# Kernel optimization log

Hardware: AMD Instinct MI355X
Metric: run time of the kernel (lower is better)

## Reference

```python
import jax, jax.numpy as jnp
import numpy as np

NUM_NODES = 50000
D_IN, D_HID, D_OUT = 128, 128, 40
NUM_EDGES = 800000


def setup_inputs() -> dict:
    key = jax.random.key(0)
    ks = jax.random.split(key, 10)
    x = jax.random.normal(ks[0], (NUM_NODES, D_IN), dtype=jnp.float32)
    edge_index = jax.random.randint(ks[1], (2, NUM_EDGES), 0, NUM_NODES, dtype=jnp.int64)
    # GCNConv weights (lin: in -> out), glorot-style init; bias init zeros per bias_init
    def glorot(k, fan_in, fan_out):
        lim = np.sqrt(6.0 / (fan_in + fan_out)).astype(np.float32)
        return jax.random.uniform(k, (fan_in, fan_out), jnp.float32, -lim, lim)
    W0 = glorot(ks[2], D_IN, D_HID)
    b0 = jnp.zeros((D_HID,), jnp.float32)
    W1 = glorot(ks[3], D_HID, D_HID)
    b1 = jnp.zeros((D_HID,), jnp.float32)
    W2 = glorot(ks[4], D_HID, D_OUT)
    b2 = jnp.zeros((D_OUT,), jnp.float32)
    return {"x": x, "edge_index": edge_index,
            "W0": W0, "b0": b0, "W1": W1, "b1": b1, "W2": W2, "b2": b2}


def _gcn_conv(h, src, dst, W, b):
    # linear projection then gather from source nodes, scatter-add to dest nodes
    hW = h @ W                                   # [N, out]
    msg = jnp.take(hW, src, axis=0)              # [E, out]
    agg = jax.ops.segment_sum(msg, dst, num_segments=NUM_NODES)  # [N, out]
    return agg + b


def reference(x, edge_index, W0, b0, W1, b1, W2, b2):
    src, dst = edge_index[0], edge_index[1]
    h = jax.nn.relu(_gcn_conv(x, src, dst, W0, b0))
    h = jax.nn.relu(_gcn_conv(h, src, dst, W1, b1))
    return _gcn_conv(h, src, dst, W2, b2)
```

## Files before the change

### kernel.cpp

```cpp
#include <hip/hip_runtime.h>

#define NN 50000
#define EE 800000

#define BKT 196
#define GB  334
#define EPB 2396
#define CAPB 6144
#define CAP 5120

typedef unsigned short u16;
typedef unsigned int u32;
typedef __attribute__((ext_vector_type(8))) short short8;
typedef __attribute__((ext_vector_type(4))) float f32x4;
typedef __attribute__((ext_vector_type(4))) unsigned short ushort4v;

__device__ __forceinline__ float b2f(u16 u) {
    return __uint_as_float(((unsigned)u) << 16);
}
__device__ __forceinline__ u16 f2b(float f) {
    unsigned u = __float_as_uint(f);
    return (u16)((u + 0x7FFF + ((u >> 16) & 1)) >> 16);
}

__global__ __launch_bounds__(256) void prep_init(
    const float* __restrict__ W0, const float* __restrict__ W1,
    const float* __restrict__ W2, u16* __restrict__ Wf,
    int* __restrict__ gCur)
{
    const int g = blockIdx.x, t = threadIdx.x;
    if (g == 24) {
        if (t < BKT) gCur[t] = t * CAPB;
        return;
    }
    int u = g * 4 + (t >> 6);
    int set = u >> 5, nt2 = (u >> 2) & 7, kt = u & 3;
    int lane = t & 63;
    const float* W = (set == 0) ? W0 : (set == 1) ? W1 : W2;
    int ld = (set == 2) ? 40 : 128;
    int ncols = (set == 2) ? 40 : 128;
    int n = nt2 * 16 + (lane & 15);
    int kb = kt * 32 + (lane >> 4) * 8;
    u16* dw = Wf + set * 16384 + (size_t)((nt2 * 4 + kt) * 64 + lane) * 8;
#pragma unroll
    for (int j = 0; j < 8; j++) {
        float v = (n < ncols) ? W[(kb + j) * ld + n] : 0.f;
        dw[j] = f2b(v);
    }
}

__global__ __launch_bounds__(256) void scatter_gemm0(
    const int* __restrict__ src, const int* __restrict__ dst,
    int* __restrict__ gCur, u32* __restrict__ pairs,
    const float* __restrict__ A, const u16* __restrict__ Wf,
    u16* __restrict__ out, int N, int E)
{
    __shared__ int cnt[BKT];
    __shared__ int cur[BKT];
    const int t = threadIdx.x;
    if (blockIdx.x < GB) {
        const int g = blockIdx.x;
        for (int b = t; b < BKT; b += 256) cnt[b] = 0;
        __syncthreads();
        const int beg = g * EPB, end = min(E, beg + EPB);
        for (int e = beg + t; e < end; e += 256)
            atomicAdd(&cnt[dst[e] >> 8], 1);
        __syncthreads();
        for (int b = t; b < BKT; b += 256)
            cur[b] = atomicAdd(&gCur[b], cnt[b]);
        __syncthreads();
        for (int e = beg + t; e < end; e += 256) {
            int d = dst[e];
            int pos = atomicAdd(&cur[d >> 8], 1);
            pairs[pos] = ((u32)src[e] << 8) | (u32)(d & 255);
        }
        return;
    }
    const int bx = blockIdx.x - GB;
    const int wave = t >> 6;
    const int lane = t & 63;
    const int m = lane & 15;
    const int q = lane >> 4;
    const int rowBase = bx * 64 + wave * 16;
    const int arow = rowBase + m;
    const bool rowOk = (arow < N);

    short8 af[4];
#pragma unroll
    for (int kt = 0; kt < 4; kt++) {
        if (rowOk) {
            float4 lo = *(const float4*)(A + (size_t)arow * 128 + kt * 32 + q * 8);
            float4 hi = *(const float4*)(A + (size_t)arow * 128 + kt * 32 + q * 8 + 4);
            short8 v;
            v[0] = (short)f2b(lo.x); v[1] = (short)f2b(lo.y);
            v[2] = (short)f2b(lo.z); v[3] = (short)f2b(lo.w);
            v[4] = (short)f2b(hi.x); v[5] = (short)f2b(hi.y);
            v[6] = (short)f2b(hi.z); v[7] = (short)f2b(hi.w);
            af[kt] = v;
        } else {
            af[kt] = (short8)0;
        }
    }

    f32x4 acc[8];
#pragma unroll
    for (int nt = 0; nt < 8; nt++) acc[nt] = (f32x4)0.f;

#pragma unroll
    for (int kt = 0; kt < 4; kt++) {
#pragma unroll
        for (int nt = 0; nt < 8; nt++) {
            short8 bf = *(const short8*)(Wf + (size_t)((nt * 4 + kt) * 64 + lane) * 8);
            acc[nt] = __builtin_amdgcn_mfma_f32_16x16x32_bf16(af[kt], bf, acc[nt], 0, 0, 0);
        }
    }

#pragma unroll
    for (int nt = 0; nt < 8; nt++) {
#pragma unroll
        for (int r = 0; r < 4; r++) {
            int orow = rowBase + q * 4 + r;
            if (orow < N) out[(size_t)orow * 128 + nt * 16 + m] = f2b(acc[nt][r]);
        }
    }
}

__global__ __launch_bounds__(256) void bucket_sort(
    const u32* __restrict__ pairs, const int* __restrict__ gCur,
    int* __restrict__ off, int* __restrict__ csr, int N, int E)
{
    __shared__ int sdeg[256];
    __shared__ int sex[256];
    __shared__ int scur[256];
    __shared__ int stage[CAP];
    const int b = blockIdx.x, t = threadIdx.x;

    int c0 = (t < BKT) ? (gCur[t] - t * CAPB) : 0;
    sex[t] = c0;
    __syncthreads();
    for (int d = 1; d < 256; d <<= 1) {
        int u = (t >= d) ? sex[t - d] : 0;
        __syncthreads();
        sex[t] += u;
        __syncthreads();
    }
    __shared__ int sBase, sCnt;
    if (t == b) { sBase = sex[t] - c0; sCnt = c0; }
    __syncthreads();
    const int base = sBase;
    const int cnt = sCnt;
    const int pbase = b * CAPB;
    __syncthreads();

    sdeg[t] = 0;
    __syncthreads();
    for (int i = t; i < cnt; i += 256)
        atomicAdd(&sdeg[pairs[pbase + i] & 255], 1);
    __syncthreads();

    int v = sdeg[t];
    sex[t] = v;
    __syncthreads();
    for (int d = 1; d < 256; d <<= 1) {
        int u = (t >= d) ? sex[t - d] : 0;
        __syncthreads();
        sex[t] += u;
        __syncthreads();
    }
    const int excl = sex[t] - v;
    const int node = b * 256 + t;
    if (node < N) off[node] = base + excl;
    if (b == BKT - 1 && t == 0) off[N] = E;
    scur[t] = excl;
    __syncthreads();

    if (cnt <= CAP) {
        for (int i = t; i < cnt; i += 256) {
            u32 p = pairs[pbase + i];
            int pos = atomicAdd(&scur[p & 255], 1);
            stage[pos] = (int)(p >> 8);
        }
        __syncthreads();
        for (int i = t; i < cnt; i += 256) csr[base + i] = stage[i];
    } else {
        for (int i = t; i < cnt; i += 256) {
            u32 p = pairs[pbase + i];
            int pos = atomicAdd(&scur[p & 255], 1);
            csr[base + pos] = (int)(p >> 8);
        }
    }
}

template<int NT, int OSTRIDE, int OCOLS>
__global__ __launch_bounds__(512) void agg_gemm_t(
    const u16* __restrict__ val, const int* __restrict__ off,
    const int* __restrict__ csr, const float* __restrict__ bias,
    const u16* __restrict__ Wf, u16* __restrict__ out, int N)
{
    __shared__ u16 A[64][136];
    const int tid = threadIdx.x;
    const int rowBase = blockIdx.x * 64;

    {
        const int c = tid & 15;
        const int nl = tid >> 4;
        float4 bA = *(const float4*)(bias + c * 8);
        float4 bB = *(const float4*)(bias + c * 8 + 4);
        float bb[8] = {bA.x, bA.y, bA.z, bA.w, bB.x, bB.y, bB.z, bB.w};
#pragma unroll
        for (int g = 0; g < 2; g++) {
            const int lrow = g * 32 + nl;
            const int node = rowBase + lrow;
            float a0[8] = {0, 0, 0, 0, 0, 0, 0, 0};
            float a1[8] = {0, 0, 0, 0, 0, 0, 0, 0};
            if (node < N) {
                const int beg = off[node], end = off[node + 1];
                int i = beg;
                for (; i + 3 < end; i += 4) {
                    int s0 = csr[i];
                    int s1 = csr[i + 1];
                    int s2 = csr[i + 2];
                    int s3 = csr[i + 3];
                    short8 v0 = *(const short8*)(val + (size_t)s0 * 128 + c * 8);
                    short8 v1 = *(const short8*)(val + (size_t)s1 * 128 + c * 8);
                    short8 v2 = *(const short8*)(val + (size_t)s2 * 128 + c * 8);
                    short8 v3 = *(const short8*)(val + (size_t)s3 * 128 + c * 8);
#pragma unroll
                    for (int j = 0; j < 8; j++) {
                        a0[j] += b2f((u16)v0[j]) + b2f((u16)v2[j]);
                        a1[j] += b2f((u16)v1[j]) + b2f((u16)v3[j]);
                    }
                }
                for (; i < end; i++) {
                    int s0 = csr[i];
                    short8 v0 = *(const short8*)(val + (size_t)s0 * 128 + c * 8);
#pragma unroll
                    for (int j = 0; j < 8; j++) a0[j] += b2f((u16)v0[j]);
                }
            }
            short8 o;
#pragma unroll
            for (int j = 0; j < 8; j++)
                o[j] = (short)f2b(fmaxf(a0[j] + a1[j] + bb[j], 0.f));
            *(short8*)&A[lrow][c * 8] = o;
        }
    }
    __syncthreads();

    const int wave = tid >> 6;
    const int lane = tid & 63;
    const int m = lane & 15;
    const int q = lane >> 4;
    const int rg = wave & 3;
    const int ch = wave >> 2;
    const int lrow = rg * 16 + m;

    short8 af[4];
#pragma unroll
    for (int kt = 0; kt < 4; kt++)
        af[kt] = *(const short8*)&A[lrow][kt * 32 + q * 8];

    constexpr int NTH = (NT + 1) / 2;
    const int ntB = ch ? NTH : 0;
    const int ntE = ch ? NT : NTH;

    f32x4 acc[NTH];
#pragma unroll
    for (int i = 0; i < NTH; i++) acc[i] = (f32x4)0.f;

#pragma unroll
    for (int kt = 0; kt < 4; kt++) {
        for (int nt = ntB; nt < ntE; nt++) {
            short8 bf = *(const short8*)(Wf + (size_t)((nt * 4 + kt) * 64 + lane) * 8);
            acc[nt - ntB] = __builtin_amdgcn_mfma_f32_16x16x32_bf16(af[kt], bf, acc[nt - ntB], 0, 0, 0);
        }
    }

    for (int nt = ntB; nt < ntE; nt++) {
        const int col = nt * 16 + m;
        if (col < OCOLS) {
#pragma unroll
            for (int r = 0; r < 4; r++) {
                int orow = rowBase + rg * 16 + q * 4 + r;
                if (orow < N) out[(size_t)orow * OSTRIDE + col] = f2b(acc[nt - ntB][r]);
            }
        }
    }
}

__global__ __launch_bounds__(256) void agg40b(
    const u16* __restrict__ val, const int* __restrict__ off,
    const int* __restrict__ csr, const float* __restrict__ b2,
    float* __restrict__ out, int N)
{
    const int c = threadIdx.x & 15;
    const int node = blockIdx.x * 16 + (threadIdx.x >> 4);
    if (node >= N || c >= 10) return;
    const int beg = off[node], end = off[node + 1];

    float a0[4] = {0, 0, 0, 0};
    float a1[4] = {0, 0, 0, 0};
    int i = beg;
    for (; i + 1 < end; i += 2) {
        int s0 = csr[i];
        int s1 = csr[i + 1];
        ushort4v v0 = *(const ushort4v*)(val + (size_t)s0 * 40 + c * 4);
        ushort4v v1 = *(const ushort4v*)(val + (size_t)s1 * 40 + c * 4);
        a0[0] += b2f(v0.x); a0[1] += b2f(v0.y); a0[2] += b2f(v0.z); a0[3] += b2f(v0.w);
        a1[0] += b2f(v1.x); a1[1] += b2f(v1.y); a1[2] += b2f(v1.z); a1[3] += b2f(v1.w);
    }
    if (i < end) {
        int s0 = csr[i];
        ushort4v v0 = *(const ushort4v*)(val + (size_t)s0 * 40 + c * 4);
        a0[0] += b2f(v0.x); a0[1] += b2f(v0.y); a0[2] += b2f(v0.z); a0[3] += b2f(v0.w);
    }
    float4 b = *(const float4*)(b2 + c * 4);
    float4 r;
    r.x = a0[0] + a1[0] + b.x;
    r.y = a0[1] + a1[1] + b.y;
    r.z = a0[2] + a1[2] + b.z;
    r.w = a0[3] + a1[3] + b.w;
    *(float4*)(out + (size_t)node * 40 + c * 4) = r;
}

extern "C" void kernel_launch(void* const* d_in, const int* in_sizes, int n_in,
                              void* d_out, int out_size, void* d_ws, size_t ws_size,
                              hipStream_t stream)
{
    const float* x  = (const float*)d_in[0];
    const int*   ei = (const int*)d_in[1];
    const float* W0 = (const float*)d_in[2];
    const float* b0 = (const float*)d_in[3];
    const float* W1 = (const float*)d_in[4];
    const float* b1 = (const float*)d_in[5];
    const float* W2 = (const float*)d_in[6];
    const float* b2 = (const float*)d_in[7];
    float* out = (float*)d_out;

    const int N = NN, E = EE;
    const int* src = ei;
    const int* dst = ei + E;

    char* ws = (char*)d_ws;
    u16* t     = (u16*)ws;
    u16* tB    = (u16*)(ws + 12800000);
    u16* t2    = (u16*)(ws + 25600000);
    u16* Wf    = (u16*)(ws + 29600000);
    int* off   = (int*)(ws + 29700000);
    int* csr   = (int*)(ws + 29900008);
    int* gCur  = (int*)(ws + 33100008);
    u32* pairs = (u32*)(ws + 33100800);

    const int tileGrid = (N + 63) / 64;
    const int agg40Grid = (N + 15) / 16;

    prep_init<<<25, 256, 0, stream>>>(W0, W1, W2, Wf, gCur);
    scatter_gemm0<<<GB + tileGrid, 256, 0, stream>>>(src, dst, gCur, pairs,
                                                     x, Wf, t, N, E);
    bucket_sort<<<BKT, 256, 0, stream>>>(pairs, gCur, off, csr, N, E);

    agg_gemm_t<8, 128, 128><<<tileGrid, 512, 0, stream>>>(t, off, csr, b0,
                                                          Wf + 16384, tB, N);
    agg_gemm_t<3, 40, 40><<<tileGrid, 512, 0, stream>>>(tB, off, csr, b1,
                                                        Wf + 32768, t2, N);
    agg40b<<<agg40Grid, 256, 0, stream>>>(t2, off, csr, b2, out, N);
}
```

Before: 209.2 us.

## Sort CSR neighbors by source range and unroll gather loops deeper

The bucket sort now keys each edge by destination plus the high bits of the source index (2048 sub-buckets), so each node's neighbor list comes out roughly ordered by source. Gathers then walk memory in a more local pattern and should hit cache more often. The aggregation loops in the 128-wide and 40-wide kernels are also unrolled to 8 and 4 neighbors, putting more independent loads in flight. The costs are larger shared-memory histograms, a per-thread 8-way local scan, and more registers in the aggregation kernels, which may lower occupancy.

```diff
diff --git a/kernel.cpp b/kernel.cpp
--- a/kernel.cpp
+++ b/kernel.cpp
@@ -129,55 +129,62 @@
     const u32* __restrict__ pairs, const int* __restrict__ gCur,
     int* __restrict__ off, int* __restrict__ csr, int N, int E)
 {
-    __shared__ int sdeg[256];
-    __shared__ int sex[256];
-    __shared__ int scur[256];
+    __shared__ int sdeg[2048];
+    __shared__ int scur[2048];
+    __shared__ int sA[256];
     __shared__ int stage[CAP];
     const int b = blockIdx.x, t = threadIdx.x;
 
     int c0 = (t < BKT) ? (gCur[t] - t * CAPB) : 0;
-    sex[t] = c0;
+    sA[t] = c0;
     __syncthreads();
     for (int d = 1; d < 256; d <<= 1) {
-        int u = (t >= d) ? sex[t - d] : 0;
-        __syncthreads();
-        sex[t] += u;
+        int u = (t >= d) ? sA[t - d] : 0;
+        __syncthreads();
+        sA[t] += u;
         __syncthreads();
     }
     __shared__ int sBase, sCnt;
-    if (t == b) { sBase = sex[t] - c0; sCnt = c0; }
+    if (t == b) { sBase = sA[t] - c0; sCnt = c0; }
     __syncthreads();
     const int base = sBase;
     const int cnt = sCnt;
     const int pbase = b * CAPB;
-    __syncthreads();
-
-    sdeg[t] = 0;
-    __syncthreads();
-    for (int i = t; i < cnt; i += 256)
-        atomicAdd(&sdeg[pairs[pbase + i] & 255], 1);
-    __syncthreads();
-
-    int v = sdeg[t];
-    sex[t] = v;
+
+    for (int k = t; k < 2048; k += 256) sdeg[k] = 0;
+    __syncthreads();
+    for (int i = t; i < cnt; i += 256) {
+        u32 p = pairs[pbase + i];
+        int key = ((p & 255) << 3) | (int)(p >> 21);
+        atomicAdd(&sdeg[key], 1);
+    }
+    __syncthreads();
+
+    int loc[8];
+    int tsum = 0;
+#pragma unroll
+    for (int j = 0; j < 8; j++) { loc[j] = tsum; tsum += sdeg[t * 8 + j]; }
+    sA[t] = tsum;
     __syncthreads();
     for (int d = 1; d < 256; d <<= 1) {
-        int u = (t >= d) ? sex[t - d] : 0;
-        __syncthreads();
-        sex[t] += u;
-        __syncthreads();
-    }
-    const int excl = sex[t] - v;
+        int u = (t >= d) ? sA[t - d] : 0;
+        __syncthreads();
+        sA[t] += u;
+        __syncthreads();
+    }
+    const int texcl = sA[t] - tsum;
     const int node = b * 256 + t;
-    if (node < N) off[node] = base + excl;
+    if (node < N) off[node] = base + texcl;
     if (b == BKT - 1 && t == 0) off[N] = E;
-    scur[t] = excl;
+#pragma unroll
+    for (int j = 0; j < 8; j++) scur[t * 8 + j] = texcl + loc[j];
     __syncthreads();
 
     if (cnt <= CAP) {
         for (int i = t; i < cnt; i += 256) {
             u32 p = pairs[pbase + i];
-            int pos = atomicAdd(&scur[p & 255], 1);
+            int key = ((p & 255) << 3) | (int)(p >> 21);
+            int pos = atomicAdd(&scur[key], 1);
             stage[pos] = (int)(p >> 8);
         }
         __syncthreads();
@@ -185,7 +192,8 @@
     } else {
         for (int i = t; i < cnt; i += 256) {
             u32 p = pairs[pbase + i];
-            int pos = atomicAdd(&scur[p & 255], 1);
+            int key = ((p & 255) << 3) | (int)(p >> 21);
+            int pos = atomicAdd(&scur[key], 1);
             csr[base + pos] = (int)(p >> 8);
         }
     }
@@ -216,6 +224,31 @@
             if (node < N) {
                 const int beg = off[node], end = off[node + 1];
                 int i = beg;
+                for (; i + 7 < end; i += 8) {
+                    int s0 = csr[i];
+                    int s1 = csr[i + 1];
+                    int s2 = csr[i + 2];
+                    int s3 = csr[i + 3];
+                    int s4 = csr[i + 4];
+                    int s5 = csr[i + 5];
+                    int s6 = csr[i + 6];
+                    int s7 = csr[i + 7];
+                    short8 v0 = *(const short8*)(val + (size_t)s0 * 128 + c * 8);
+                    short8 v1 = *(const short8*)(val + (size_t)s1 * 128 + c * 8);
+                    short8 v2 = *(const short8*)(val + (size_t)s2 * 128 + c * 8);
+                    short8 v3 = *(const short8*)(val + (size_t)s3 * 128 + c * 8);
+                    short8 v4 = *(const short8*)(val + (size_t)s4 * 128 + c * 8);
+                    short8 v5 = *(const short8*)(val + (size_t)s5 * 128 + c * 8);
+                    short8 v6 = *(const short8*)(val + (size_t)s6 * 128 + c * 8);
+                    short8 v7 = *(const short8*)(val + (size_t)s7 * 128 + c * 8);
+#pragma unroll
+                    for (int j = 0; j < 8; j++) {
+                        a0[j] += (b2f((u16)v0[j]) + b2f((u16)v2[j]))
+                               + (b2f((u16)v4[j]) + b2f((u16)v6[j]));
+                        a1[j] += (b2f((u16)v1[j]) + b2f((u16)v3[j]))
+                               + (b2f((u16)v5[j]) + b2f((u16)v7[j]));
+                    }
+                }
                 for (; i + 3 < end; i += 4) {
                     int s0 = csr[i];
                     int s1 = csr[i + 1];
@@ -301,6 +334,20 @@
     float a0[4] = {0, 0, 0, 0};
     float a1[4] = {0, 0, 0, 0};
     int i = beg;
+    for (; i + 3 < end; i += 4) {
+        int s0 = csr[i];
+        int s1 = csr[i + 1];
+        int s2 = csr[i + 2];
+        int s3 = csr[i + 3];
+        ushort4v v0 = *(const ushort4v*)(val + (size_t)s0 * 40 + c * 4);
+        ushort4v v1 = *(const ushort4v*)(val + (size_t)s1 * 40 + c * 4);
+        ushort4v v2 = *(const ushort4v*)(val + (size_t)s2 * 40 + c * 4);
+        ushort4v v3 = *(const ushort4v*)(val + (size_t)s3 * 40 + c * 4);
+        a0[0] += b2f(v0.x) + b2f(v2.x); a0[1] += b2f(v0.y) + b2f(v2.y);
+        a0[2] += b2f(v0.z) + b2f(v2.z); a0[3] += b2f(v0.w) + b2f(v2.w);
+        a1[0] += b2f(v1.x) + b2f(v3.x); a1[1] += b2f(v1.y) + b2f(v3.y);
+        a1[2] += b2f(v1.z) + b2f(v3.z); a1[3] += b2f(v1.w) + b2f(v3.w);
+    }
     for (; i + 1 < end; i += 2) {
         int s0 = csr[i];
         int s1 = csr[i + 1];
```

Measured after the change: 215.6 us. 3.1% more time.

## Fuse all GCN stages into one cooperative persistent kernel with grid syncs

Applied to the files above, without the earlier changes.

Replaces the six kernel launches with a single cooperative persistent kernel. It runs weight prep, edge bucketing, bucket sort plus the first GEMM, the two aggregate+GEMM layers and the final aggregation as phases separated by grid.sync, with work handed out through atomic task counters. The aim is to remove launch gaps and tail bubbles between stages, and to let the sort overlap with the first GEMM. The cost is grid-wide barriers, a fixed persistent grid whose 512-thread blocks may limit occupancy, and an extra __syncthreads inside the aggregation. If the cooperative launch fails, the old launch sequence runs instead.

```diff
diff --git a/kernel.cpp b/kernel.cpp
--- a/kernel.cpp
+++ b/kernel.cpp
@@ -1,4 +1,7 @@
 #include <hip/hip_runtime.h>
+#include <hip/hip_cooperative_groups.h>
+
+namespace cg = cooperative_groups;
 
 #define NN 50000
 #define EE 800000
@@ -8,6 +11,10 @@
 #define EPB 2396
 #define CAPB 6144
 #define CAP 5120
+#define NTHR 512
+#define G0TILES 391
+#define L1TILES 782
+#define AGG40T 1563
 
 typedef unsigned short u16;
 typedef unsigned int u32;
@@ -21,6 +28,334 @@
 __device__ __forceinline__ u16 f2b(float f) {
     unsigned u = __float_as_uint(f);
     return (u16)((u + 0x7FFF + ((u >> 16) & 1)) >> 16);
+}
+
+union alignas(16) LdsU {
+    struct { int sdeg[256]; int sex[256]; int scur[256]; int stage[CAP]; } so;
+    struct { int cnt[BKT]; int cur[BKT]; } sc;
+    u16 A[64][136];
+};
+
+template<int NT, int OST, int OC>
+__device__ __forceinline__ void agg_tile(
+    int task, int tid, const u16* __restrict__ val, const int* __restrict__ off,
+    const int* __restrict__ csr, const float* __restrict__ bias,
+    const u16* __restrict__ Wfs, u16* __restrict__ outp, int N, LdsU* L)
+{
+    const int rowBase = task * 64;
+    {
+        const int c8 = tid & 7;
+        const int nl = tid >> 3;
+        const int node = rowBase + nl;
+        const bool ok = (node < N);
+        const int beg = ok ? off[node] : 0;
+        const int end = ok ? off[node + 1] : 0;
+#pragma unroll
+        for (int pass = 0; pass < 2; pass++) {
+            const int cb = pass * 64 + c8 * 8;
+            float4 bA = *(const float4*)(bias + cb);
+            float4 bB = *(const float4*)(bias + cb + 4);
+            float bb[8] = {bA.x, bA.y, bA.z, bA.w, bB.x, bB.y, bB.z, bB.w};
+            float a0[8] = {0, 0, 0, 0, 0, 0, 0, 0};
+            float a1[8] = {0, 0, 0, 0, 0, 0, 0, 0};
+            int i = beg;
+            for (; i + 3 < end; i += 4) {
+                int s0 = csr[i];
+                int s1 = csr[i + 1];
+                int s2 = csr[i + 2];
+                int s3 = csr[i + 3];
+                short8 v0 = *(const short8*)(val + (size_t)s0 * 128 + cb);
+                short8 v1 = *(const short8*)(val + (size_t)s1 * 128 + cb);
+                short8 v2 = *(const short8*)(val + (size_t)s2 * 128 + cb);
+                short8 v3 = *(const short8*)(val + (size_t)s3 * 128 + cb);
+#pragma unroll
+                for (int j = 0; j < 8; j++) {
+                    a0[j] += b2f((u16)v0[j]) + b2f((u16)v2[j]);
+                    a1[j] += b2f((u16)v1[j]) + b2f((u16)v3[j]);
+                }
+            }
+            for (; i < end; i++) {
+                int s0 = csr[i];
+                short8 v0 = *(const short8*)(val + (size_t)s0 * 128 + cb);
+#pragma unroll
+                for (int j = 0; j < 8; j++) a0[j] += b2f((u16)v0[j]);
+            }
+            short8 o;
+#pragma unroll
+            for (int j = 0; j < 8; j++)
+                o[j] = (short)f2b(fmaxf(a0[j] + a1[j] + bb[j], 0.f));
+            *(short8*)&L->A[nl][cb] = o;
+            __syncthreads();
+        }
+    }
+    const int wave = tid >> 6;
+    const int lane = tid & 63;
+    const int m = lane & 15;
+    const int q = lane >> 4;
+    const int rg = wave & 3;
+    const int ch = wave >> 2;
+    const int lrow = rg * 16 + m;
+
+    short8 af[4];
+#pragma unroll
+    for (int kt = 0; kt < 4; kt++)
+        af[kt] = *(const short8*)&L->A[lrow][kt * 32 + q * 8];
+    __syncthreads();
+
+    constexpr int NTH = (NT + 1) / 2;
+    const int ntB = ch ? NTH : 0;
+    const int ntE = ch ? NT : NTH;
+
+    f32x4 acc[NTH];
+#pragma unroll
+    for (int i2 = 0; i2 < NTH; i2++) acc[i2] = (f32x4)0.f;
+
+#pragma unroll
+    for (int kt = 0; kt < 4; kt++) {
+        for (int nt = ntB; nt < ntE; nt++) {
+            short8 bf = *(const short8*)(Wfs + (size_t)((nt * 4 + kt) * 64 + lane) * 8);
+            acc[nt - ntB] = __builtin_amdgcn_mfma_f32_16x16x32_bf16(af[kt], bf, acc[nt - ntB], 0, 0, 0);
+        }
+    }
+
+    for (int nt = ntB; nt < ntE; nt++) {
+        const int col = nt * 16 + m;
+        if (col < OC) {
+#pragma unroll
+            for (int r = 0; r < 4; r++) {
+                int orow = rowBase + rg * 16 + q * 4 + r;
+                if (orow < N)
+                    __builtin_nontemporal_store((u16)f2b(acc[nt - ntB][r]),
+                                                &outp[(size_t)orow * OST + col]);
+            }
+        }
+    }
+}
+
+__global__ __launch_bounds__(NTHR, 4) void mega(
+    const float* __restrict__ x, const int* __restrict__ esrc,
+    const int* __restrict__ edst,
+    const float* __restrict__ W0, const float* __restrict__ b0,
+    const float* __restrict__ W1, const float* __restrict__ b1,
+    const float* __restrict__ W2, const float* __restrict__ b2p,
+    u16* __restrict__ Wf, int* __restrict__ gCur, u32* __restrict__ pairs,
+    int* __restrict__ off, int* __restrict__ csr,
+    u16* __restrict__ h0, u16* __restrict__ h1, u16* __restrict__ h2,
+    float* __restrict__ outp, int* __restrict__ phCtr, int N, int E)
+{
+    cg::grid_group grid = cg::this_grid();
+    __shared__ LdsU L;
+    __shared__ int sBase, sCnt, sTask;
+    const int tid = threadIdx.x;
+
+    for (int task = blockIdx.x; task < 13; task += gridDim.x) {
+        if (task < 12) {
+            int u = task * 8 + (tid >> 6);
+            int set = u >> 5, nt2 = (u >> 2) & 7, kt = u & 3;
+            int lane = tid & 63;
+            const float* W = (set == 0) ? W0 : (set == 1) ? W1 : W2;
+            int ld = (set == 2) ? 40 : 128;
+            int ncols = (set == 2) ? 40 : 128;
+            int n = nt2 * 16 + (lane & 15);
+            int kb = kt * 32 + (lane >> 4) * 8;
+            u16* dw = Wf + set * 16384 + (size_t)((nt2 * 4 + kt) * 64 + lane) * 8;
+#pragma unroll
+            for (int j = 0; j < 8; j++) {
+                float v = (n < ncols) ? W[(kb + j) * ld + n] : 0.f;
+                dw[j] = f2b(v);
+            }
+        } else {
+            if (tid < BKT) gCur[tid] = tid * CAPB;
+            if (tid >= 256 && tid < 260) phCtr[tid - 256] = 0;
+        }
+    }
+    grid.sync();
+
+    for (int task = blockIdx.x; task < GB; task += gridDim.x) {
+        for (int b = tid; b < BKT; b += NTHR) L.sc.cnt[b] = 0;
+        __syncthreads();
+        const int beg = task * EPB, end = min(E, beg + EPB);
+        for (int e = beg + tid; e < end; e += NTHR)
+            atomicAdd(&L.sc.cnt[edst[e] >> 8], 1);
+        __syncthreads();
+        for (int b = tid; b < BKT; b += NTHR)
+            L.sc.cur[b] = atomicAdd(&gCur[b], L.sc.cnt[b]);
+        __syncthreads();
+        for (int e = beg + tid; e < end; e += NTHR) {
+            int d = edst[e];
+            int pos = atomicAdd(&L.sc.cur[d >> 8], 1);
+            pairs[pos] = ((u32)esrc[e] << 8) | (u32)(d & 255);
+        }
+        __syncthreads();
+    }
+    grid.sync();
+
+    for (;;) {
+        if (tid == 0) sTask = atomicAdd(&phCtr[0], 1);
+        __syncthreads();
+        const int task = sTask;
+        __syncthreads();
+        if (task >= BKT + G0TILES) break;
+        if (task < BKT) {
+            const int b = task;
+            int c0 = 0;
+            if (tid < 256) {
+                c0 = (tid < BKT) ? (gCur[tid] - tid * CAPB) : 0;
+                L.so.sex[tid] = c0;
+            }
+            __syncthreads();
+            for (int d = 1; d < 256; d <<= 1) {
+                int u = (tid >= d && tid < 256) ? L.so.sex[tid - d] : 0;
+                __syncthreads();
+                if (tid < 256) L.so.sex[tid] += u;
+                __syncthreads();
+            }
+            if (tid == b) { sBase = L.so.sex[tid] - c0; sCnt = c0; }
+            __syncthreads();
+            const int base = sBase, cnt = sCnt, pbase = b * CAPB;
+            if (tid < 256) L.so.sdeg[tid] = 0;
+            __syncthreads();
+            for (int i = tid; i < cnt; i += NTHR)
+                atomicAdd(&L.so.sdeg[pairs[pbase + i] & 255], 1);
+            __syncthreads();
+            int v = 0;
+            if (tid < 256) { v = L.so.sdeg[tid]; L.so.sex[tid] = v; }
+            __syncthreads();
+            for (int d = 1; d < 256; d <<= 1) {
+                int u = (tid >= d && tid < 256) ? L.so.sex[tid - d] : 0;
+                __syncthreads();
+                if (tid < 256) L.so.sex[tid] += u;
+                __syncthreads();
+            }
+            if (tid < 256) {
+                const int excl = L.so.sex[tid] - v;
+                const int node = b * 256 + tid;
+                if (node < N) off[node] = base + excl;
+                L.so.scur[tid] = excl;
+            }
+            if (b == BKT - 1 && tid == 0) off[N] = E;
+            __syncthreads();
+            if (cnt <= CAP) {
+                for (int i = tid; i < cnt; i += NTHR) {
+                    u32 p = pairs[pbase + i];
+                    int pos = atomicAdd(&L.so.scur[p & 255], 1);
+                    L.so.stage[pos] = (int)(p >> 8);
+                }
+                __syncthreads();
+                for (int i = tid; i < cnt; i += NTHR) csr[base + i] = L.so.stage[i];
+            } else {
+                for (int i = tid; i < cnt; i += NTHR) {
+                    u32 p = pairs[pbase + i];
+                    int pos = atomicAdd(&L.so.scur[p & 255], 1);
+                    csr[base + pos] = (int)(p >> 8);
+                }
+            }
+            __syncthreads();
+        } else {
+            const int bx = task - BKT;
+            const int wave = tid >> 6;
+            const int lane = tid & 63;
+            const int m = lane & 15;
+            const int q = lane >> 4;
+            const int rowBase = bx * 128 + wave * 16;
+            const int arow = rowBase + m;
+            const bool rowOk = (arow < N);
+            short8 af[4];
+#pragma unroll
+            for (int kt = 0; kt < 4; kt++) {
+                if (rowOk) {
+                    float4 lo = *(const float4*)(x + (size_t)arow * 128 + kt * 32 + q * 8);
+                    float4 hi = *(const float4*)(x + (size_t)arow * 128 + kt * 32 + q * 8 + 4);
+                    short8 vv;
+                    vv[0] = (short)f2b(lo.x); vv[1] = (short)f2b(lo.y);
+                    vv[2] = (short)f2b(lo.z); vv[3] = (short)f2b(lo.w);
+                    vv[4] = (short)f2b(hi.x); vv[5] = (short)f2b(hi.y);
+                    vv[6] = (short)f2b(hi.z); vv[7] = (short)f2b(hi.w);
+                    af[kt] = vv;
+                } else {
+                    af[kt] = (short8)0;
+                }
+            }
+            f32x4 acc[8];
+#pragma unroll
+            for (int nt = 0; nt < 8; nt++) acc[nt] = (f32x4)0.f;
+#pragma unroll
+            for (int kt = 0; kt < 4; kt++) {
+#pragma unroll
+                for (int nt = 0; nt < 8; nt++) {
+                    short8 bf = *(const short8*)(Wf + (size_t)((nt * 4 + kt) * 64 + lane) * 8);
+                    acc[nt] = __builtin_amdgcn_mfma_f32_16x16x32_bf16(af[kt], bf, acc[nt], 0, 0, 0);
+                }
+            }
+#pragma unroll
+            for (int nt = 0; nt < 8; nt++) {
+#pragma unroll
+                for (int r = 0; r < 4; r++) {
+                    int orow = rowBase + q * 4 + r;
+                    if (orow < N)
+                        __builtin_nontemporal_store((u16)f2b(acc[nt][r]),
+                                                    &h0[(size_t)orow * 128 + nt * 16 + m]);
+                }
+            }
+        }
+    }
+    grid.sync();
+
+    for (;;) {
+        if (tid == 0) sTask = atomicAdd(&phCtr[1], 1);
+        __syncthreads();
+        const int task = sTask;
+        __syncthreads();
+        if (task >= L1TILES) break;
+        agg_tile<8, 128, 128>(task, tid, h0, off, csr, b0, Wf + 16384, h1, N, &L);
+    }
+    grid.sync();
+
+    for (;;) {
+        if (tid == 0) sTask = atomicAdd(&phCtr[2], 1);
+        __syncthreads();
+        const int task = sTask;
+        __syncthreads();
+        if (task >= L1TILES) break;
+        agg_tile<3, 40, 40>(task, tid, h1, off, csr, b1, Wf + 32768, h2, N, &L);
+    }
+    grid.sync();
+
+    for (;;) {
+        if (tid == 0) sTask = atomicAdd(&phCtr[3], 1);
+        __syncthreads();
+        const int task = sTask;
+        __syncthreads();
+        if (task >= AGG40T) break;
+        const int c = tid & 15;
+        const int node = task * 32 + (tid >> 4);
+        if (node < N && c < 10) {
+            const int beg = off[node], end = off[node + 1];
+            float a0[4] = {0, 0, 0, 0};
+            float a1[4] = {0, 0, 0, 0};
+            int i = beg;
+            for (; i + 1 < end; i += 2) {
+                int s0 = csr[i];
+                int s1 = csr[i + 1];
+                ushort4v v0 = *(const ushort4v*)(h2 + (size_t)s0 * 40 + c * 4);
+                ushort4v v1 = *(const ushort4v*)(h2 + (size_t)s1 * 40 + c * 4);
+                a0[0] += b2f(v0.x); a0[1] += b2f(v0.y); a0[2] += b2f(v0.z); a0[3] += b2f(v0.w);
+                a1[0] += b2f(v1.x); a1[1] += b2f(v1.y); a1[2] += b2f(v1.z); a1[3] += b2f(v1.w);
+            }
+            if (i < end) {
+                int s0 = csr[i];
+                ushort4v v0 = *(const ushort4v*)(h2 + (size_t)s0 * 40 + c * 4);
+                a0[0] += b2f(v0.x); a0[1] += b2f(v0.y); a0[2] += b2f(v0.z); a0[3] += b2f(v0.w);
+            }
+            float4 bv = *(const float4*)(b2p + c * 4);
+            float4 r;
+            r.x = a0[0] + a1[0] + bv.x;
+            r.y = a0[1] + a1[1] + bv.y;
+            r.z = a0[2] + a1[2] + bv.z;
+            r.w = a0[3] + a1[3] + bv.w;
+            *(float4*)(outp + (size_t)node * 40 + c * 4) = r;
+        }
+    }
 }
 
 __global__ __launch_bounds__(256) void prep_init(
@@ -101,11 +436,9 @@
             af[kt] = (short8)0;
         }
     }
-
     f32x4 acc[8];
 #pragma unroll
     for (int nt = 0; nt < 8; nt++) acc[nt] = (f32x4)0.f;
-
 #pragma unroll
     for (int kt = 0; kt < 4; kt++) {
 #pragma unroll
@@ -114,7 +447,6 @@
             acc[nt] = __builtin_amdgcn_mfma_f32_16x16x32_bf16(af[kt], bf, acc[nt], 0, 0, 0);
         }
     }
-
 #pragma unroll
     for (int nt = 0; nt < 8; nt++) {
 #pragma unroll
@@ -200,7 +532,6 @@
     __shared__ u16 A[64][136];
     const int tid = threadIdx.x;
     const int rowBase = blockIdx.x * 64;
-
     {
         const int c = tid & 15;
         const int nl = tid >> 4;
@@ -246,7 +577,6 @@
         }
     }
     __syncthreads();
-
     const int wave = tid >> 6;
     const int lane = tid & 63;
     const int m = lane & 15;
@@ -254,20 +584,16 @@
     const int rg = wave & 3;
     const int ch = wave >> 2;
     const int lrow = rg * 16 + m;
-
     short8 af[4];
 #pragma unroll
     for (int kt = 0; kt < 4; kt++)
         af[kt] = *(const short8*)&A[lrow][kt * 32 + q * 8];
-
     constexpr int NTH = (NT + 1) / 2;
     const int ntB = ch ? NTH : 0;
     const int ntE = ch ? NT : NTH;
-
     f32x4 acc[NTH];
 #pragma unroll
     for (int i = 0; i < NTH; i++) acc[i] = (f32x4)0.f;
-
 #pragma unroll
     for (int kt = 0; kt < 4; kt++) {
         for (int nt = ntB; nt < ntE; nt++) {
@@ -275,7 +601,6 @@
             acc[nt - ntB] = __builtin_amdgcn_mfma_f32_16x16x32_bf16(af[kt], bf, acc[nt - ntB], 0, 0, 0);
         }
     }
-
     for (int nt = ntB; nt < ntE; nt++) {
         const int col = nt * 16 + m;
         if (col < OCOLS) {
@@ -297,7 +622,6 @@
     const int node = blockIdx.x * 16 + (threadIdx.x >> 4);
     if (node >= N || c >= 10) return;
     const int beg = off[node], end = off[node + 1];
-
     float a0[4] = {0, 0, 0, 0};
     float a1[4] = {0, 0, 0, 0};
     int i = beg;
@@ -337,31 +661,50 @@
     const float* b2 = (const float*)d_in[7];
     float* out = (float*)d_out;
 
-    const int N = NN, E = EE;
+    int N = NN, E = EE;
     const int* src = ei;
     const int* dst = ei + E;
 
     char* ws = (char*)d_ws;
-    u16* t     = (u16*)ws;
-    u16* tB    = (u16*)(ws + 12800000);
-    u16* t2    = (u16*)(ws + 25600000);
+    u16* h0    = (u16*)ws;
+    u16* h1    = (u16*)(ws + 12800000);
+    u16* h2    = (u16*)(ws + 25600000);
     u16* Wf    = (u16*)(ws + 29600000);
     int* off   = (int*)(ws + 29700000);
     int* csr   = (int*)(ws + 29900008);
     int* gCur  = (int*)(ws + 33100008);
     u32* pairs = (u32*)(ws + 33100800);
-
-    const int tileGrid = (N + 63) / 64;
-    const int agg40Grid = (N + 15) / 16;
-
-    prep_init<<<25, 256, 0, stream>>>(W0, W1, W2, Wf, gCur);
-    scatter_gemm0<<<GB + tileGrid, 256, 0, stream>>>(src, dst, gCur, pairs,
-                                                     x, Wf, t, N, E);
-    bucket_sort<<<BKT, 256, 0, stream>>>(pairs, gCur, off, csr, N, E);
-
-    agg_gemm_t<8, 128, 128><<<tileGrid, 512, 0, stream>>>(t, off, csr, b0,
-                                                          Wf + 16384, tB, N);
-    agg_gemm_t<3, 40, 40><<<tileGrid, 512, 0, stream>>>(tB, off, csr, b1,
-                                                        Wf + 32768, t2, N);
-    agg40b<<<agg40Grid, 256, 0, stream>>>(t2, off, csr, b2, out, N);
-}
+    int* phCtr = (int*)(ws + 37920000);
+
+    int maxb = 0;
+    hipError_t oe = hipOccupancyMaxActiveBlocksPerMultiprocessor(
+        &maxb, (const void*)mega, NTHR, 0);
+    int nblk = 256;
+    if (oe == hipSuccess && maxb >= 1) {
+        nblk = maxb * 256;
+        if (nblk > 512) nblk = 512;
+    }
+
+    void* args[] = {(void*)&x, (void*)&src, (void*)&dst,
+                    (void*)&W0, (void*)&b0, (void*)&W1, (void*)&b1,
+                    (void*)&W2, (void*)&b2,
+                    (void*)&Wf, (void*)&gCur, (void*)&pairs,
+                    (void*)&off, (void*)&csr,
+                    (void*)&h0, (void*)&h1, (void*)&h2,
+                    (void*)&out, (void*)&phCtr, (void*)&N, (void*)&E};
+
+    if (hipLaunchCooperativeKernel((const void*)mega, dim3(nblk), dim3(NTHR),
+                                   args, 0, stream) != hipSuccess) {
+        const int tileGrid = (N + 63) / 64;
+        const int agg40Grid = (N + 15) / 16;
+        prep_init<<<25, 256, 0, stream>>>(W0, W1, W2, Wf, gCur);
+        scatter_gemm0<<<GB + tileGrid, 256, 0, stream>>>(src, dst, gCur, pairs,
+                                                         x, Wf, h0, N, E);
+        bucket_sort<<<BKT, 256, 0, stream>>>(pairs, gCur, off, csr, N, E);
+        agg_gemm_t<8, 128, 128><<<tileGrid, 512, 0, stream>>>(h0, off, csr, b0,
+                                                              Wf + 16384, h1, N);
+        agg_gemm_t<3, 40, 40><<<tileGrid, 512, 0, stream>>>(h1, off, csr, b1,
+                                                            Wf + 32768, h2, N);
+        agg40b<<<agg40Grid, 256, 0, stream>>>(h2, off, csr, b2, out, N);
+    }
+}
```

New measurement: 465.9 us. +122.7%, slower.
